# Kernel tuning notes

Measured on AMD Instinct MI355X. Metric: run time of the kernel, lower is better.

The kernel has to match this reference:

```python
import jax, jax.numpy as jnp
import numpy as np

B, NINP, NCLS = 16384, 2048, 100


def setup_inputs() -> dict:
    key = jax.random.key(0)
    k1, k2, k3, k4, k5 = jax.random.split(key, 5)
    s = 1.0 / np.sqrt(NINP)
    return {
        "time_series": jax.random.normal(k1, (B, NINP), jnp.float32),
        "w_weight": jax.random.uniform(k2, (NINP, NINP), jnp.float32, -s, s),
        "w_bias": jax.random.uniform(k3, (NINP,), jnp.float32, -s, s),
        "fc_weight": jax.random.uniform(k4, (NCLS, NINP), jnp.float32, -s, s),
        "fc_bias": jax.random.uniform(k5, (NCLS,), jnp.float32, -s, s),
    }


def reference(time_series, w_weight, w_bias, fc_weight, fc_bias):
    # time_series: [B, N]
    n = time_series.shape[1]
    # gamma = cumsum(softmax(w(x), axis=1), axis=1): monotone warp in (0, 1]
    gamma = jnp.cumsum(jax.nn.softmax(time_series @ w_weight.T + w_bias, axis=1), axis=1)
    # Interp1d(linspace(0,1,N), x, gamma): per-row linear interpolation,
    # sampling each series at the warped time points gamma.
    xs = jnp.linspace(0.0, 1.0, n, dtype=time_series.dtype)  # shared knot grid
    warped = jax.vmap(lambda g, y: jnp.interp(g, xs, y))(gamma, time_series)  # [B, N]
    return warped @ fc_weight.T + fc_bias  # [B, nclasses]
```

## Files before the change

### kernel.cpp

```cpp
#include <hip/hip_runtime.h>
#include <hip/hip_bf16.h>

#define BROWS 16384
#define NDIM  2048
#define NCLS  100

typedef __attribute__((ext_vector_type(8))) __bf16 bf16x8;
typedef __attribute__((ext_vector_type(4))) float f32x4;
typedef __attribute__((ext_vector_type(4))) unsigned short u16x4;
typedef __attribute__((ext_vector_type(8))) unsigned short u16x8;

__device__ __forceinline__ unsigned short f2bf(float f) {
    union { float f; unsigned int u; } v; v.f = f;
    unsigned int u = v.u;
    unsigned int r = (u + 0x7fffu + ((u >> 16) & 1u)) >> 16;
    return (unsigned short)r;
}
__device__ __forceinline__ float bf2f(unsigned short h) {
    union { unsigned int u; float f; } v; v.u = ((unsigned int)h) << 16;
    return v.f;
}

#define GLOAD_LDS(g, l) \
    __builtin_amdgcn_global_load_lds((const __attribute__((address_space(1))) void*)(g), \
                                     (__attribute__((address_space(3))) void*)(l), 16, 0, 0)

__global__ __launch_bounds__(256) void split_kernel(const float4* __restrict__ src,
                                                    u16x4* __restrict__ hi,
                                                    u16x4* __restrict__ lo, int n4)
{
    int i = blockIdx.x * 256 + threadIdx.x;
    if (i >= n4) return;
    float4 v = src[i];
    u16x4 h, l;
    h.x = f2bf(v.x); l.x = f2bf(v.x - bf2f(h.x));
    h.y = f2bf(v.y); l.y = f2bf(v.y - bf2f(h.y));
    h.z = f2bf(v.z); l.z = f2bf(v.z - bf2f(h.z));
    h.w = f2bf(v.w); l.w = f2bf(v.w - bf2f(h.w));
    hi[i] = h; lo[i] = l;
}

__global__ __launch_bounds__(256) void cvt_bf16_kernel(const float4* __restrict__ src,
                                                       u16x4* __restrict__ dst, int n4)
{
    int i = blockIdx.x * 256 + threadIdx.x;
    if (i >= n4) return;
    float4 v = src[i];
    u16x4 h;
    h.x = f2bf(v.x); h.y = f2bf(v.y); h.z = f2bf(v.z); h.w = f2bf(v.w);
    dst[i] = h;
}

__global__ __launch_bounds__(256) void gemm1_mfma_fused_kernel(
        const unsigned short* __restrict__ xhi,
        const unsigned short* __restrict__ xlo,
        const unsigned short* __restrict__ whi,
        const unsigned short* __restrict__ wlo,
        const float* __restrict__ bias,
        float* __restrict__ C)
{
    __shared__ unsigned short sAh[128 * 32];
    __shared__ unsigned short sAl[128 * 32];
    __shared__ unsigned short sBh[128 * 32];
    __shared__ unsigned short sBl[128 * 32];

    const int tid  = threadIdx.x;
    const int lane = tid & 63;
    const int w    = tid >> 6;
    const int wm   = w & 1;
    const int wn   = w >> 1;
    const int m0   = blockIdx.y * 128;
    const int n0   = blockIdx.x * 128;

    const int c0 = w * 128 + lane;
    const int r0 = c0 >> 2;
    const int q0 = (c0 & 3) ^ ((r0 >> 1) & 3);
    const int c1 = c0 + 64;
    const int r1 = c1 >> 2;
    const int q1 = (c1 & 3) ^ ((r1 >> 1) & 3);

    const size_t a_goff0 = (size_t)(m0 + r0) * NDIM + q0 * 8;
    const size_t a_goff1 = (size_t)(m0 + r1) * NDIM + q1 * 8;
    const size_t b_goff0 = (size_t)(n0 + r0) * NDIM + q0 * 8;
    const size_t b_goff1 = (size_t)(n0 + r1) * NDIM + q1 * 8;

    unsigned short* ldsAh0 = &sAh[w * 1024];   unsigned short* ldsAh1 = &sAh[w * 1024 + 512];
    unsigned short* ldsAl0 = &sAl[w * 1024];   unsigned short* ldsAl1 = &sAl[w * 1024 + 512];
    unsigned short* ldsBh0 = &sBh[w * 1024];   unsigned short* ldsBh1 = &sBh[w * 1024 + 512];
    unsigned short* ldsBl0 = &sBl[w * 1024];   unsigned short* ldsBl1 = &sBl[w * 1024 + 512];

    const int lm = lane & 15;
    const int lk = lane >> 4;
    int offA[4], offB[4];
#pragma unroll
    for (int i = 0; i < 4; i++) {
        int ra = wm * 64 + i * 16 + lm;
        offA[i] = ra * 32 + ((lk ^ ((ra >> 1) & 3)) * 8);
        int rb = wn * 64 + i * 16 + lm;
        offB[i] = rb * 32 + ((lk ^ ((rb >> 1) & 3)) * 8);
    }

    f32x4 acc[4][4];
#pragma unroll
    for (int i = 0; i < 4; i++)
#pragma unroll
        for (int j = 0; j < 4; j++) acc[i][j] = (f32x4){0.f, 0.f, 0.f, 0.f};

    for (int kt = 0; kt < NDIM; kt += 32) {
        GLOAD_LDS(xhi + a_goff0 + kt, ldsAh0);
        GLOAD_LDS(xhi + a_goff1 + kt, ldsAh1);
        GLOAD_LDS(xlo + a_goff0 + kt, ldsAl0);
        GLOAD_LDS(xlo + a_goff1 + kt, ldsAl1);
        GLOAD_LDS(whi + b_goff0 + kt, ldsBh0);
        GLOAD_LDS(whi + b_goff1 + kt, ldsBh1);
        GLOAD_LDS(wlo + b_goff0 + kt, ldsBl0);
        GLOAD_LDS(wlo + b_goff1 + kt, ldsBl1);
        __syncthreads();

        bf16x8 ah[4], al[4], bh[4], bl[4];
#pragma unroll
        for (int i = 0; i < 4; i++) {
            ah[i] = *(const bf16x8*)&sAh[offA[i]];
            al[i] = *(const bf16x8*)&sAl[offA[i]];
            bh[i] = *(const bf16x8*)&sBh[offB[i]];
            bl[i] = *(const bf16x8*)&sBl[offB[i]];
        }
#pragma unroll
        for (int i = 0; i < 4; i++)
#pragma unroll
            for (int j = 0; j < 4; j++) {
                acc[i][j] = __builtin_amdgcn_mfma_f32_16x16x32_bf16(ah[i], bh[j], acc[i][j], 0, 0, 0);
                acc[i][j] = __builtin_amdgcn_mfma_f32_16x16x32_bf16(ah[i], bl[j], acc[i][j], 0, 0, 0);
                acc[i][j] = __builtin_amdgcn_mfma_f32_16x16x32_bf16(al[i], bh[j], acc[i][j], 0, 0, 0);
            }
        __syncthreads();
    }

    const int cn = lane & 15;
    const int rg = lane >> 4;
    float bb[4];
#pragma unroll
    for (int j = 0; j < 4; j++) bb[j] = bias[n0 + wn * 64 + j * 16 + cn];
#pragma unroll
    for (int i = 0; i < 4; i++) {
#pragma unroll
        for (int j = 0; j < 4; j++) {
            const int n = n0 + wn * 64 + j * 16 + cn;
#pragma unroll
            for (int reg = 0; reg < 4; reg++) {
                const int m = m0 + wm * 64 + i * 16 + rg * 4 + reg;
                C[(size_t)m * NDIM + n] = acc[i][j][reg] + bb[j];
            }
        }
    }
}

__global__ __launch_bounds__(256) void warp_bf16_kernel(const float* __restrict__ X,
                                                        const float* __restrict__ L,
                                                        unsigned short* __restrict__ Wout)
{
    const int N = NDIM;
    const int row = blockIdx.x;
    const int tid = threadIdx.x;
    const int lane = tid & 63;
    const int wave = tid >> 6;

    __shared__ float s_x[NDIM];
    __shared__ float s_red[4];
    __shared__ float s_wsum[4];

    const float* lrow = L + (size_t)row * N;
    const float* xrow = X + (size_t)row * N;

    float v[8];
    {
        float4 l0 = *(const float4*)(lrow + tid * 8);
        float4 l1 = *(const float4*)(lrow + tid * 8 + 4);
        v[0] = l0.x; v[1] = l0.y; v[2] = l0.z; v[3] = l0.w;
        v[4] = l1.x; v[5] = l1.y; v[6] = l1.z; v[7] = l1.w;
        float4 x0 = *(const float4*)(xrow + tid * 8);
        float4 x1 = *(const float4*)(xrow + tid * 8 + 4);
        *(float4*)&s_x[tid * 8]     = x0;
        *(float4*)&s_x[tid * 8 + 4] = x1;
    }

    float mx = v[0];
#pragma unroll
    for (int j = 1; j < 8; j++) mx = fmaxf(mx, v[j]);
#pragma unroll
    for (int off = 32; off > 0; off >>= 1) mx = fmaxf(mx, __shfl_down(mx, off));
    if (lane == 0) s_red[wave] = mx;
    __syncthreads();
    mx = fmaxf(fmaxf(s_red[0], s_red[1]), fmaxf(s_red[2], s_red[3]));

    float c = 0.0f;
#pragma unroll
    for (int j = 0; j < 8; j++) {
        float e = __expf(v[j] - mx);
        c += e;
        v[j] = c;
    }

    float sc = c;
#pragma unroll
    for (int off = 1; off < 64; off <<= 1) {
        float t = __shfl_up(sc, off);
        if (lane >= off) sc += t;
    }
    if (lane == 63) s_wsum[wave] = sc;
    __syncthreads();
    float base = 0.0f, total = 0.0f;
#pragma unroll
    for (int w = 0; w < 4; w++) {
        float t = s_wsum[w];
        if (w < wave) base += t;
        total += t;
    }
    const float inv = 1.0f / total;
    const float prefix = base + (sc - c);

    u16x8 o;
#pragma unroll
    for (int j = 0; j < 8; j++) {
        float g = (prefix + v[j]) * inv;
        float pos = g * (float)(N - 1);
        pos = fminf(fmaxf(pos, 0.0f), (float)(N - 1));
        int i = (int)pos;
        if (i > N - 2) i = N - 2;
        float f = pos - (float)i;
        o[j] = f2bf(fmaf(f, s_x[i + 1] - s_x[i], s_x[i]));
    }
    *(u16x8*)(Wout + (size_t)row * N + tid * 8) = o;
}

__global__ __launch_bounds__(256) void gemm2_mfma_kernel(
        const unsigned short* __restrict__ Wp,
        const unsigned short* __restrict__ F,
        const float* __restrict__ fb,
        float* __restrict__ out)
{
    __shared__ unsigned short sA[64 * 32];
    __shared__ unsigned short sB[128 * 32];

    const int tid  = threadIdx.x;
    const int lane = tid & 63;
    const int w    = tid >> 6;
    const int wm   = w & 1;
    const int wn   = w >> 1;
    const int m0   = blockIdx.x * 64;

    const int ca = w * 64 + lane;
    const int ra = ca >> 2;
    const int qa = (ca & 3) ^ ((ra >> 1) & 3);
    const size_t a_goff = (size_t)(m0 + ra) * NDIM + qa * 8;
    unsigned short* ldsA = &sA[w * 512];

    const int cb0 = w * 128 + lane;
    const int rb0 = cb0 >> 2;
    const int qb0 = (cb0 & 3) ^ ((rb0 >> 1) & 3);
    const int cb1 = cb0 + 64;
    const int rb1 = cb1 >> 2;
    const int qb1 = (cb1 & 3) ^ ((rb1 >> 1) & 3);
    const size_t b_goff0 = (size_t)(rb0 < NCLS ? rb0 : NCLS - 1) * NDIM + qb0 * 8;
    const size_t b_goff1 = (size_t)(rb1 < NCLS ? rb1 : NCLS - 1) * NDIM + qb1 * 8;
    unsigned short* ldsB0 = &sB[w * 1024];
    unsigned short* ldsB1 = &sB[w * 1024 + 512];

    const int lm = lane & 15;
    const int lk = lane >> 4;
    int offA[2], offB[4];
#pragma unroll
    for (int i = 0; i < 2; i++) {
        int r = wm * 32 + i * 16 + lm;
        offA[i] = r * 32 + ((lk ^ ((r >> 1) & 3)) * 8);
    }
#pragma unroll
    for (int j = 0; j < 4; j++) {
        int r = wn * 64 + j * 16 + lm;
        offB[j] = r * 32 + ((lk ^ ((r >> 1) & 3)) * 8);
    }

    f32x4 acc[2][4];
#pragma unroll
    for (int i = 0; i < 2; i++)
#pragma unroll
        for (int j = 0; j < 4; j++) acc[i][j] = (f32x4){0.f, 0.f, 0.f, 0.f};

    for (int kt = 0; kt < NDIM; kt += 32) {
        GLOAD_LDS(Wp + a_goff + kt, ldsA);
        GLOAD_LDS(F + b_goff0 + kt, ldsB0);
        GLOAD_LDS(F + b_goff1 + kt, ldsB1);
        __syncthreads();

        bf16x8 af[2], bf[4];
#pragma unroll
        for (int i = 0; i < 2; i++) af[i] = *(const bf16x8*)&sA[offA[i]];
#pragma unroll
        for (int j = 0; j < 4; j++) bf[j] = *(const bf16x8*)&sB[offB[j]];
#pragma unroll
        for (int i = 0; i < 2; i++)
#pragma unroll
            for (int j = 0; j < 4; j++)
                acc[i][j] = __builtin_amdgcn_mfma_f32_16x16x32_bf16(af[i], bf[j], acc[i][j], 0, 0, 0);
        __syncthreads();
    }

    const int cn = lane & 15;
    const int rg = lane >> 4;
#pragma unroll
    for (int i = 0; i < 2; i++) {
#pragma unroll
        for (int j = 0; j < 4; j++) {
            const int n = wn * 64 + j * 16 + cn;
            if (n < NCLS) {
                const float bbn = fb[n];
#pragma unroll
                for (int reg = 0; reg < 4; reg++) {
                    const int m = m0 + wm * 32 + i * 16 + rg * 4 + reg;
                    out[(size_t)m * NCLS + n] = acc[i][j][reg] + bbn;
                }
            }
        }
    }
}

__global__ __launch_bounds__(256) void gemm1_kernel(const float* __restrict__ X,
                                                    const float* __restrict__ W,
                                                    const float* __restrict__ bias,
                                                    float* __restrict__ C)
{
    const int K = NDIM;
    __shared__ float sA[16][128];
    __shared__ float sB[16][128];
    const int tid = threadIdx.x;
    const int tx = tid & 15;
    const int ty = tid >> 4;
    const int m0 = blockIdx.y * 128;
    const int n0 = blockIdx.x * 128;
    float acc[8][8];
#pragma unroll
    for (int i = 0; i < 8; i++)
#pragma unroll
        for (int j = 0; j < 8; j++) acc[i][j] = 0.0f;
    const int s_m = tid >> 1;
    const int s_c = (tid & 1) * 8;
    const float* Ag = X + (size_t)(m0 + s_m) * K + s_c;
    const float* Bg = W + (size_t)(n0 + s_m) * K + s_c;
    for (int kt = 0; kt < K; kt += 16) {
        float4 av0 = *(const float4*)(Ag + kt);
        float4 av1 = *(const float4*)(Ag + kt + 4);
        float4 bv0 = *(const float4*)(Bg + kt);
        float4 bv1 = *(const float4*)(Bg + kt + 4);
        __syncthreads();
        sA[s_c + 0][s_m] = av0.x; sA[s_c + 1][s_m] = av0.y;
        sA[s_c + 2][s_m] = av0.z; sA[s_c + 3][s_m] = av0.w;
        sA[s_c + 4][s_m] = av1.x; sA[s_c + 5][s_m] = av1.y;
        sA[s_c + 6][s_m] = av1.z; sA[s_c + 7][s_m] = av1.w;
        sB[s_c + 0][s_m] = bv0.x; sB[s_c + 1][s_m] = bv0.y;
        sB[s_c + 2][s_m] = bv0.z; sB[s_c + 3][s_m] = bv0.w;
        sB[s_c + 4][s_m] = bv1.x; sB[s_c + 5][s_m] = bv1.y;
        sB[s_c + 6][s_m] = bv1.z; sB[s_c + 7][s_m] = bv1.w;
        __syncthreads();
#pragma unroll
        for (int k = 0; k < 16; k++) {
            float4 a0 = *(const float4*)&sA[k][ty * 8];
            float4 a1 = *(const float4*)&sA[k][ty * 8 + 4];
            float4 b0 = *(const float4*)&sB[k][tx * 8];
            float4 b1 = *(const float4*)&sB[k][tx * 8 + 4];
            float a[8] = {a0.x, a0.y, a0.z, a0.w, a1.x, a1.y, a1.z, a1.w};
            float b[8] = {b0.x, b0.y, b0.z, b0.w, b1.x, b1.y, b1.z, b1.w};
#pragma unroll
            for (int i = 0; i < 8; i++)
#pragma unroll
                for (int j = 0; j < 8; j++)
                    acc[i][j] = fmaf(a[i], b[j], acc[i][j]);
        }
    }
    float bb[8];
#pragma unroll
    for (int j = 0; j < 8; j++) bb[j] = bias[n0 + tx * 8 + j];
#pragma unroll
    for (int i = 0; i < 8; i++) {
        const int m = m0 + ty * 8 + i;
        float* crow = C + (size_t)m * NDIM + n0 + tx * 8;
        *(float4*)(crow)     = make_float4(acc[i][0] + bb[0], acc[i][1] + bb[1],
                                           acc[i][2] + bb[2], acc[i][3] + bb[3]);
        *(float4*)(crow + 4) = make_float4(acc[i][4] + bb[4], acc[i][5] + bb[5],
                                           acc[i][6] + bb[6], acc[i][7] + bb[7]);
    }
}

__global__ __launch_bounds__(256) void warp_kernel_f32(const float* __restrict__ X,
                                                       float* __restrict__ L)
{
    const int N = NDIM;
    const int row = blockIdx.x;
    const int tid = threadIdx.x;
    const int lane = tid & 63;
    const int wave = tid >> 6;
    __shared__ float s_x[NDIM];
    __shared__ float s_red[4];
    __shared__ float s_wsum[4];
    float* lrow = L + (size_t)row * N;
    const float* xrow = X + (size_t)row * N;
    float v[8];
    {
        float4 l0 = *(const float4*)(lrow + tid * 8);
        float4 l1 = *(const float4*)(lrow + tid * 8 + 4);
        v[0] = l0.x; v[1] = l0.y; v[2] = l0.z; v[3] = l0.w;
        v[4] = l1.x; v[5] = l1.y; v[6] = l1.z; v[7] = l1.w;
        float4 x0 = *(const float4*)(xrow + tid * 8);
        float4 x1 = *(const float4*)(xrow + tid * 8 + 4);
        *(float4*)&s_x[tid * 8]     = x0;
        *(float4*)&s_x[tid * 8 + 4] = x1;
    }
    float mx = v[0];
#pragma unroll
    for (int j = 1; j < 8; j++) mx = fmaxf(mx, v[j]);
#pragma unroll
    for (int off = 32; off > 0; off >>= 1) mx = fmaxf(mx, __shfl_down(mx, off));
    if (lane == 0) s_red[wave] = mx;
    __syncthreads();
    mx = fmaxf(fmaxf(s_red[0], s_red[1]), fmaxf(s_red[2], s_red[3]));
    float c = 0.0f;
#pragma unroll
    for (int j = 0; j < 8; j++) {
        float e = __expf(v[j] - mx);
        c += e;
        v[j] = c;
    }
    float sc = c;
#pragma unroll
    for (int off = 1; off < 64; off <<= 1) {
        float t = __shfl_up(sc, off);
        if (lane >= off) sc += t;
    }
    if (lane == 63) s_wsum[wave] = sc;
    __syncthreads();
    float base = 0.0f, total = 0.0f;
#pragma unroll
    for (int w = 0; w < 4; w++) {
        float t = s_wsum[w];
        if (w < wave) base += t;
        total += t;
    }
    const float inv = 1.0f / total;
    const float prefix = base + (sc - c);
    float w8[8];
#pragma unroll
    for (int j = 0; j < 8; j++) {
        float g = (prefix + v[j]) * inv;
        float pos = g * (float)(N - 1);
        pos = fminf(fmaxf(pos, 0.0f), (float)(N - 1));
        int i = (int)pos;
        if (i > N - 2) i = N - 2;
        float f = pos - (float)i;
        w8[j] = fmaf(f, s_x[i + 1] - s_x[i], s_x[i]);
    }
    *(float4*)(lrow + tid * 8)     = make_float4(w8[0], w8[1], w8[2], w8[3]);
    *(float4*)(lrow + tid * 8 + 4) = make_float4(w8[4], w8[5], w8[6], w8[7]);
}

__global__ __launch_bounds__(256) void gemm2_kernel(const float* __restrict__ Wp,
                                                    const float* __restrict__ F,
                                                    const float* __restrict__ fb,
                                                    float* __restrict__ out)
{
    const int K = NDIM;
    __shared__ float sA[16][64];
    __shared__ float sB[16][128];
    const int tid = threadIdx.x;
    const int tx = tid & 15;
    const int ty = tid >> 4;
    const int m0 = blockIdx.x * 64;
    float acc[4][8];
#pragma unroll
    for (int i = 0; i < 4; i++)
#pragma unroll
        for (int j = 0; j < 8; j++) acc[i][j] = 0.0f;
    const int a_m = tid >> 2;
    const int a_c = (tid & 3) * 4;
    const int b_n = tid >> 1;
    const int b_c = (tid & 1) * 8;
    const bool bvalid = (b_n < NCLS);
    const float* Ag = Wp + (size_t)(m0 + a_m) * K + a_c;
    const float* Bg = F + (size_t)b_n * K + b_c;
    for (int kt = 0; kt < K; kt += 16) {
        float4 av = *(const float4*)(Ag + kt);
        float4 bv0 = make_float4(0.f, 0.f, 0.f, 0.f);
        float4 bv1 = make_float4(0.f, 0.f, 0.f, 0.f);
        if (bvalid) {
            bv0 = *(const float4*)(Bg + kt);
            bv1 = *(const float4*)(Bg + kt + 4);
        }
        __syncthreads();
        sA[a_c + 0][a_m] = av.x; sA[a_c + 1][a_m] = av.y;
        sA[a_c + 2][a_m] = av.z; sA[a_c + 3][a_m] = av.w;
        sB[b_c + 0][b_n] = bv0.x; sB[b_c + 1][b_n] = bv0.y;
        sB[b_c + 2][b_n] = bv0.z; sB[b_c + 3][b_n] = bv0.w;
        sB[b_c + 4][b_n] = bv1.x; sB[b_c + 5][b_n] = bv1.y;
        sB[b_c + 6][b_n] = bv1.z; sB[b_c + 7][b_n] = bv1.w;
        __syncthreads();
#pragma unroll
        for (int k = 0; k < 16; k++) {
            float4 a4 = *(const float4*)&sA[k][ty * 4];
            float4 b0 = *(const float4*)&sB[k][tx * 8];
            float4 b1 = *(const float4*)&sB[k][tx * 8 + 4];
            float a[4] = {a4.x, a4.y, a4.z, a4.w};
            float b[8] = {b0.x, b0.y, b0.z, b0.w, b1.x, b1.y, b1.z, b1.w};
#pragma unroll
            for (int i = 0; i < 4; i++)
#pragma unroll
                for (int j = 0; j < 8; j++)
                    acc[i][j] = fmaf(a[i], b[j], acc[i][j]);
        }
    }
#pragma unroll
    for (int i = 0; i < 4; i++) {
        const int m = m0 + ty * 4 + i;
#pragma unroll
        for (int j = 0; j < 8; j++) {
            const int n = tx * 8 + j;
            if (n < NCLS) out[(size_t)m * NCLS + n] = acc[i][j] + fb[n];
        }
    }
}

extern "C" void kernel_launch(void* const* d_in, const int* in_sizes, int n_in,
                              void* d_out, int out_size, void* d_ws, size_t ws_size,
                              hipStream_t stream) {
    const float* x  = (const float*)d_in[0];
    const float* ww = (const float*)d_in[1];
    const float* wb = (const float*)d_in[2];
    const float* fw = (const float*)d_in[3];
    const float* fb = (const float*)d_in[4];
    float* out = (float*)d_out;

    char* ws = (char*)d_ws;
    float* logits = (float*)ws;
    const size_t LOGITS_B = (size_t)BROWS * NDIM * 4;
    const size_t XBF_B    = (size_t)BROWS * NDIM * 2;
    const size_t WBF_B    = (size_t)NDIM * NDIM * 2;
    unsigned short* xhi = (unsigned short*)(ws + LOGITS_B);
    unsigned short* xlo = (unsigned short*)(ws + LOGITS_B + XBF_B);
    unsigned short* whi = (unsigned short*)(ws + LOGITS_B + 2 * XBF_B);
    unsigned short* wlo = (unsigned short*)(ws + LOGITS_B + 2 * XBF_B + WBF_B);
    unsigned short* wbf = xlo;
    unsigned short* fwb = wlo;
    const size_t WS_NEED = LOGITS_B + 2 * XBF_B + 2 * WBF_B;

    if (ws_size >= WS_NEED) {
        split_kernel<<<(BROWS * NDIM / 4 + 255) / 256, 256, 0, stream>>>(
            (const float4*)x, (u16x4*)xhi, (u16x4*)xlo, BROWS * NDIM / 4);
        split_kernel<<<(NDIM * NDIM / 4 + 255) / 256, 256, 0, stream>>>(
            (const float4*)ww, (u16x4*)whi, (u16x4*)wlo, NDIM * NDIM / 4);
        gemm1_mfma_fused_kernel<<<dim3(NDIM / 128, BROWS / 128), 256, 0, stream>>>(
            xhi, xlo, whi, wlo, wb, logits);
        warp_bf16_kernel<<<BROWS, 256, 0, stream>>>(x, logits, wbf);
        cvt_bf16_kernel<<<(NCLS * NDIM / 4 + 255) / 256, 256, 0, stream>>>(
            (const float4*)fw, (u16x4*)fwb, NCLS * NDIM / 4);
        gemm2_mfma_kernel<<<BROWS / 64, 256, 0, stream>>>(wbf, fwb, fb, out);
    } else {
        gemm1_kernel<<<dim3(NDIM / 128, BROWS / 128), 256, 0, stream>>>(x, ww, wb, logits);
        warp_kernel_f32<<<BROWS, 256, 0, stream>>>(x, logits);
        gemm2_kernel<<<BROWS / 64, 256, 0, stream>>>(logits, fw, fb, out);
    }
}
```

Measured before the change: 699.2 us.

## Use 32x32 MFMA in gemm1, retile gemm2, merge split kernels

Gemm1 switches from 16x16x32 to 32x32x16 bf16 MFMA tiles, with two k-substeps per 32-wide LDS tile. This lowers LDS fragment reads per MFMA and uses the larger-output instruction. Gemm2 moves to a 32-row M tile with a 64-wide K step and an 8-way swizzle, doubling the grid and halving the barrier count. The two fp32-to-bf16 hi/lo split launches are merged into one kernel. Risk: register pressure from the 16-wide accumulators, and correctness of the new output index mapping.

```diff
diff --git a/kernel.cpp b/kernel.cpp
--- a/kernel.cpp
+++ b/kernel.cpp
@@ -7,6 +7,7 @@
 
 typedef __attribute__((ext_vector_type(8))) __bf16 bf16x8;
 typedef __attribute__((ext_vector_type(4))) float f32x4;
+typedef __attribute__((ext_vector_type(16))) float f32x16;
 typedef __attribute__((ext_vector_type(4))) unsigned short u16x4;
 typedef __attribute__((ext_vector_type(8))) unsigned short u16x8;
 
@@ -25,19 +26,23 @@
     __builtin_amdgcn_global_load_lds((const __attribute__((address_space(1))) void*)(g), \
                                      (__attribute__((address_space(3))) void*)(l), 16, 0, 0)
 
-__global__ __launch_bounds__(256) void split_kernel(const float4* __restrict__ src,
-                                                    u16x4* __restrict__ hi,
-                                                    u16x4* __restrict__ lo, int n4)
+__global__ __launch_bounds__(256) void prep_kernel(const float4* __restrict__ x,
+                                                   const float4* __restrict__ w,
+                                                   u16x4* __restrict__ xhi, u16x4* __restrict__ xlo,
+                                                   u16x4* __restrict__ whi, u16x4* __restrict__ wlo,
+                                                   int n4x, int n4w)
 {
     int i = blockIdx.x * 256 + threadIdx.x;
-    if (i >= n4) return;
-    float4 v = src[i];
+    const float4* src; u16x4 *hi, *lo; int idx;
+    if (i < n4x) { src = x; hi = xhi; lo = xlo; idx = i; }
+    else { idx = i - n4x; if (idx >= n4w) return; src = w; hi = whi; lo = wlo; }
+    float4 v = src[idx];
     u16x4 h, l;
     h.x = f2bf(v.x); l.x = f2bf(v.x - bf2f(h.x));
     h.y = f2bf(v.y); l.y = f2bf(v.y - bf2f(h.y));
     h.z = f2bf(v.z); l.z = f2bf(v.z - bf2f(h.z));
     h.w = f2bf(v.w); l.w = f2bf(v.w - bf2f(h.w));
-    hi[i] = h; lo[i] = l;
+    hi[idx] = h; lo[idx] = l;
 }
 
 __global__ __launch_bounds__(256) void cvt_bf16_kernel(const float4* __restrict__ src,
@@ -89,22 +94,27 @@
     unsigned short* ldsBh0 = &sBh[w * 1024];   unsigned short* ldsBh1 = &sBh[w * 1024 + 512];
     unsigned short* ldsBl0 = &sBl[w * 1024];   unsigned short* ldsBl1 = &sBl[w * 1024 + 512];
 
-    const int lm = lane & 15;
-    const int lk = lane >> 4;
-    int offA[4], offB[4];
-#pragma unroll
-    for (int i = 0; i < 4; i++) {
-        int ra = wm * 64 + i * 16 + lm;
-        offA[i] = ra * 32 + ((lk ^ ((ra >> 1) & 3)) * 8);
-        int rb = wn * 64 + i * 16 + lm;
-        offB[i] = rb * 32 + ((lk ^ ((rb >> 1) & 3)) * 8);
-    }
-
-    f32x4 acc[4][4];
-#pragma unroll
-    for (int i = 0; i < 4; i++)
-#pragma unroll
-        for (int j = 0; j < 4; j++) acc[i][j] = (f32x4){0.f, 0.f, 0.f, 0.f};
+    const int ln32 = lane & 31;
+    const int lk2  = lane >> 5;
+    int offA[2][2], offB[2][2];
+#pragma unroll
+    for (int i = 0; i < 2; i++) {
+#pragma unroll
+        for (int ks = 0; ks < 2; ks++) {
+            int ra = wm * 64 + i * 32 + ln32;
+            offA[i][ks] = ra * 32 + (((2 * ks + lk2) ^ ((ra >> 1) & 3)) * 8);
+            int rb = wn * 64 + i * 32 + ln32;
+            offB[i][ks] = rb * 32 + (((2 * ks + lk2) ^ ((rb >> 1) & 3)) * 8);
+        }
+    }
+
+    f32x16 acc[2][2];
+#pragma unroll
+    for (int i = 0; i < 2; i++)
+#pragma unroll
+        for (int j = 0; j < 2; j++)
+#pragma unroll
+            for (int r = 0; r < 16; r++) acc[i][j][r] = 0.f;
 
     for (int kt = 0; kt < NDIM; kt += 32) {
         GLOAD_LDS(xhi + a_goff0 + kt, ldsAh0);
@@ -117,38 +127,39 @@
         GLOAD_LDS(wlo + b_goff1 + kt, ldsBl1);
         __syncthreads();
 
-        bf16x8 ah[4], al[4], bh[4], bl[4];
-#pragma unroll
-        for (int i = 0; i < 4; i++) {
-            ah[i] = *(const bf16x8*)&sAh[offA[i]];
-            al[i] = *(const bf16x8*)&sAl[offA[i]];
-            bh[i] = *(const bf16x8*)&sBh[offB[i]];
-            bl[i] = *(const bf16x8*)&sBl[offB[i]];
-        }
-#pragma unroll
-        for (int i = 0; i < 4; i++)
-#pragma unroll
-            for (int j = 0; j < 4; j++) {
-                acc[i][j] = __builtin_amdgcn_mfma_f32_16x16x32_bf16(ah[i], bh[j], acc[i][j], 0, 0, 0);
-                acc[i][j] = __builtin_amdgcn_mfma_f32_16x16x32_bf16(ah[i], bl[j], acc[i][j], 0, 0, 0);
-                acc[i][j] = __builtin_amdgcn_mfma_f32_16x16x32_bf16(al[i], bh[j], acc[i][j], 0, 0, 0);
+#pragma unroll
+        for (int ks = 0; ks < 2; ks++) {
+            bf16x8 ah[2], al[2], bh[2], bl[2];
+#pragma unroll
+            for (int i = 0; i < 2; i++) {
+                ah[i] = *(const bf16x8*)&sAh[offA[i][ks]];
+                al[i] = *(const bf16x8*)&sAl[offA[i][ks]];
+                bh[i] = *(const bf16x8*)&sBh[offB[i][ks]];
+                bl[i] = *(const bf16x8*)&sBl[offB[i][ks]];
             }
-        __syncthreads();
-    }
-
-    const int cn = lane & 15;
-    const int rg = lane >> 4;
-    float bb[4];
-#pragma unroll
-    for (int j = 0; j < 4; j++) bb[j] = bias[n0 + wn * 64 + j * 16 + cn];
-#pragma unroll
-    for (int i = 0; i < 4; i++) {
-#pragma unroll
-        for (int j = 0; j < 4; j++) {
-            const int n = n0 + wn * 64 + j * 16 + cn;
-#pragma unroll
-            for (int reg = 0; reg < 4; reg++) {
-                const int m = m0 + wm * 64 + i * 16 + rg * 4 + reg;
+#pragma unroll
+            for (int i = 0; i < 2; i++)
+#pragma unroll
+                for (int j = 0; j < 2; j++) {
+                    acc[i][j] = __builtin_amdgcn_mfma_f32_32x32x16_bf16(ah[i], bh[j], acc[i][j], 0, 0, 0);
+                    acc[i][j] = __builtin_amdgcn_mfma_f32_32x32x16_bf16(ah[i], bl[j], acc[i][j], 0, 0, 0);
+                    acc[i][j] = __builtin_amdgcn_mfma_f32_32x32x16_bf16(al[i], bh[j], acc[i][j], 0, 0, 0);
+                }
+        }
+        __syncthreads();
+    }
+
+    float bb[2];
+#pragma unroll
+    for (int j = 0; j < 2; j++) bb[j] = bias[n0 + wn * 64 + j * 32 + ln32];
+#pragma unroll
+    for (int i = 0; i < 2; i++) {
+#pragma unroll
+        for (int j = 0; j < 2; j++) {
+            const int n = n0 + wn * 64 + j * 32 + ln32;
+#pragma unroll
+            for (int reg = 0; reg < 16; reg++) {
+                const int m = m0 + wm * 64 + i * 32 + (reg & 3) + 8 * (reg >> 2) + 4 * lk2;
                 C[(size_t)m * NDIM + n] = acc[i][j][reg] + bb[j];
             }
         }
@@ -239,86 +250,83 @@
         const float* __restrict__ fb,
         float* __restrict__ out)
 {
-    __shared__ unsigned short sA[64 * 32];
-    __shared__ unsigned short sB[128 * 32];
+    __shared__ unsigned short sA[32 * 64];
+    __shared__ unsigned short sB[128 * 64];
 
     const int tid  = threadIdx.x;
     const int lane = tid & 63;
     const int w    = tid >> 6;
     const int wm   = w & 1;
     const int wn   = w >> 1;
-    const int m0   = blockIdx.x * 64;
+    const int m0   = blockIdx.x * 32;
 
     const int ca = w * 64 + lane;
-    const int ra = ca >> 2;
-    const int qa = (ca & 3) ^ ((ra >> 1) & 3);
+    const int ra = ca >> 3;
+    const int qa = (ca & 7) ^ (ra & 7);
     const size_t a_goff = (size_t)(m0 + ra) * NDIM + qa * 8;
     unsigned short* ldsA = &sA[w * 512];
 
-    const int cb0 = w * 128 + lane;
-    const int rb0 = cb0 >> 2;
-    const int qb0 = (cb0 & 3) ^ ((rb0 >> 1) & 3);
-    const int cb1 = cb0 + 64;
-    const int rb1 = cb1 >> 2;
-    const int qb1 = (cb1 & 3) ^ ((rb1 >> 1) & 3);
-    const size_t b_goff0 = (size_t)(rb0 < NCLS ? rb0 : NCLS - 1) * NDIM + qb0 * 8;
-    const size_t b_goff1 = (size_t)(rb1 < NCLS ? rb1 : NCLS - 1) * NDIM + qb1 * 8;
-    unsigned short* ldsB0 = &sB[w * 1024];
-    unsigned short* ldsB1 = &sB[w * 1024 + 512];
+    size_t b_goff[4];
+    unsigned short* ldsB[4];
+#pragma unroll
+    for (int t = 0; t < 4; t++) {
+        const int cb = t * 256 + w * 64 + lane;
+        const int rb = cb >> 3;
+        const int qb = (cb & 7) ^ (rb & 7);
+        b_goff[t] = (size_t)(rb < NCLS ? rb : NCLS - 1) * NDIM + qb * 8;
+        ldsB[t] = &sB[(size_t)t * 2048 + w * 512];
+    }
 
     const int lm = lane & 15;
     const int lk = lane >> 4;
-    int offA[2], offB[4];
-#pragma unroll
-    for (int i = 0; i < 2; i++) {
-        int r = wm * 32 + i * 16 + lm;
-        offA[i] = r * 32 + ((lk ^ ((r >> 1) & 3)) * 8);
-    }
-#pragma unroll
-    for (int j = 0; j < 4; j++) {
-        int r = wn * 64 + j * 16 + lm;
-        offB[j] = r * 32 + ((lk ^ ((r >> 1) & 3)) * 8);
-    }
-
-    f32x4 acc[2][4];
-#pragma unroll
-    for (int i = 0; i < 2; i++)
-#pragma unroll
-        for (int j = 0; j < 4; j++) acc[i][j] = (f32x4){0.f, 0.f, 0.f, 0.f};
-
-    for (int kt = 0; kt < NDIM; kt += 32) {
+    int offA[2], offB[4][2];
+#pragma unroll
+    for (int ks = 0; ks < 2; ks++) {
+        int r = wm * 16 + lm;
+        offA[ks] = r * 64 + (((4 * ks + lk) ^ (r & 7)) * 8);
+    }
+#pragma unroll
+    for (int j = 0; j < 4; j++)
+#pragma unroll
+        for (int ks = 0; ks < 2; ks++) {
+            int r = wn * 64 + j * 16 + lm;
+            offB[j][ks] = r * 64 + (((4 * ks + lk) ^ (r & 7)) * 8);
+        }
+
+    f32x4 acc[4];
+#pragma unroll
+    for (int j = 0; j < 4; j++) acc[j] = (f32x4){0.f, 0.f, 0.f, 0.f};
+
+    for (int kt = 0; kt < NDIM; kt += 64) {
         GLOAD_LDS(Wp + a_goff + kt, ldsA);
-        GLOAD_LDS(F + b_goff0 + kt, ldsB0);
-        GLOAD_LDS(F + b_goff1 + kt, ldsB1);
-        __syncthreads();
-
-        bf16x8 af[2], bf[4];
-#pragma unroll
-        for (int i = 0; i < 2; i++) af[i] = *(const bf16x8*)&sA[offA[i]];
-#pragma unroll
-        for (int j = 0; j < 4; j++) bf[j] = *(const bf16x8*)&sB[offB[j]];
-#pragma unroll
-        for (int i = 0; i < 2; i++)
+#pragma unroll
+        for (int t = 0; t < 4; t++) GLOAD_LDS(F + b_goff[t] + kt, ldsB[t]);
+        __syncthreads();
+
+#pragma unroll
+        for (int ks = 0; ks < 2; ks++) {
+            bf16x8 af = *(const bf16x8*)&sA[offA[ks]];
+            bf16x8 bf[4];
+#pragma unroll
+            for (int j = 0; j < 4; j++) bf[j] = *(const bf16x8*)&sB[offB[j][ks]];
 #pragma unroll
             for (int j = 0; j < 4; j++)
-                acc[i][j] = __builtin_amdgcn_mfma_f32_16x16x32_bf16(af[i], bf[j], acc[i][j], 0, 0, 0);
+                acc[j] = __builtin_amdgcn_mfma_f32_16x16x32_bf16(af, bf[j], acc[j], 0, 0, 0);
+        }
         __syncthreads();
     }
 
     const int cn = lane & 15;
     const int rg = lane >> 4;
 #pragma unroll
-    for (int i = 0; i < 2; i++) {
-#pragma unroll
-        for (int j = 0; j < 4; j++) {
-            const int n = wn * 64 + j * 16 + cn;
-            if (n < NCLS) {
-                const float bbn = fb[n];
-#pragma unroll
-                for (int reg = 0; reg < 4; reg++) {
-                    const int m = m0 + wm * 32 + i * 16 + rg * 4 + reg;
-                    out[(size_t)m * NCLS + n] = acc[i][j][reg] + bbn;
-                }
+    for (int j = 0; j < 4; j++) {
+        const int n = wn * 64 + j * 16 + cn;
+        if (n < NCLS) {
+            const float bbn = fb[n];
+#pragma unroll
+            for (int reg = 0; reg < 4; reg++) {
+                const int m = m0 + wm * 16 + rg * 4 + reg;
+                out[(size_t)m * NCLS + n] = acc[j][reg] + bbn;
             }
         }
     }
@@ -550,16 +558,17 @@
     const size_t WS_NEED = LOGITS_B + 2 * XBF_B + 2 * WBF_B;
 
     if (ws_size >= WS_NEED) {
-        split_kernel<<<(BROWS * NDIM / 4 + 255) / 256, 256, 0, stream>>>(
-            (const float4*)x, (u16x4*)xhi, (u16x4*)xlo, BROWS * NDIM / 4);
-        split_kernel<<<(NDIM * NDIM / 4 + 255) / 256, 256, 0, stream>>>(
-            (const float4*)ww, (u16x4*)whi, (u16x4*)wlo, NDIM * NDIM / 4);
+        const int n4x = BROWS * NDIM / 4;
+        const int n4w = NDIM * NDIM / 4;
+        prep_kernel<<<(n4x + n4w + 255) / 256, 256, 0, stream>>>(
+            (const float4*)x, (const float4*)ww,
+            (u16x4*)xhi, (u16x4*)xlo, (u16x4*)whi, (u16x4*)wlo, n4x, n4w);
         gemm1_mfma_fused_kernel<<<dim3(NDIM / 128, BROWS / 128), 256, 0, stream>>>(
             xhi, xlo, whi, wlo, wb, logits);
         warp_bf16_kernel<<<BROWS, 256, 0, stream>>>(x, logits, wbf);
         cvt_bf16_kernel<<<(NCLS * NDIM / 4 + 255) / 256, 256, 0, stream>>>(
             (const float4*)fw, (u16x4*)fwb, NCLS * NDIM / 4);
-        gemm2_mfma_kernel<<<BROWS / 64, 256, 0, stream>>>(wbf, fwb, fb, out);
+        gemm2_mfma_kernel<<<BROWS / 32, 256, 0, stream>>>(wbf, fwb, fb, out);
     } else {
         gemm1_kernel<<<dim3(NDIM / 128, BROWS / 128), 256, 0, stream>>>(x, ww, wb, logits);
         warp_kernel_f32<<<BROWS, 256, 0, stream>>>(x, logits);
```

New measurement: 699.6 us. Within noise of the previous version (+0.0%).
